# Kernel optimization log

Hardware: AMD Instinct MI355X
Metric: run time of the kernel (lower is better)

Reference implementation:

```python
import jax, jax.numpy as jnp
import numpy as np

N_HEADS = 16
GROUP_SIZE = 4
D_MODEL = 2048
N_GROUPS = N_HEADS // GROUP_SIZE  # 4 KV heads
HEAD_DIM = D_MODEL // N_HEADS     # 128
B, S = 2, 2048


def setup_inputs() -> dict:
    key = jax.random.key(0)
    ks = jax.random.split(key, 10)
    sd = 1.0 / np.sqrt(D_MODEL)
    inp = {
        "x": jax.random.normal(ks[0], (B, S, D_MODEL), dtype=jnp.float32),
        # per-position, per-pair rotation angles (llama-style freqs)
        "rotary_freqs": jax.random.uniform(ks[1], (S, HEAD_DIM // 2), dtype=jnp.float32) * 6.283,
        # weights stored as [in, out] so forward is x @ W + b
        "Wq": jax.random.normal(ks[2], (D_MODEL, D_MODEL), dtype=jnp.float32) * sd,
        "bq": jnp.zeros((D_MODEL,), dtype=jnp.float32),
        "Wk": jax.random.normal(ks[3], (D_MODEL, N_GROUPS * HEAD_DIM), dtype=jnp.float32) * sd,
        "bk": jnp.zeros((N_GROUPS * HEAD_DIM,), dtype=jnp.float32),
        "Wv": jax.random.normal(ks[4], (D_MODEL, N_GROUPS * HEAD_DIM), dtype=jnp.float32) * sd,
        "bv": jnp.zeros((N_GROUPS * HEAD_DIM,), dtype=jnp.float32),
        "Wo": jax.random.normal(ks[5], (D_MODEL, D_MODEL), dtype=jnp.float32) * sd,
        "bo": jnp.zeros((D_MODEL,), dtype=jnp.float32),
    }
    return inp


def _rope(t, cos, sin):
    # t: [B, S, H, head_dim]; cos/sin: [1, S, 1, head_dim//2]
    t2 = t.reshape(t.shape[:-1] + (HEAD_DIM // 2, 2))
    te, to = t2[..., 0], t2[..., 1]
    re = te * cos - to * sin
    ro = te * sin + to * cos
    return jnp.stack([re, ro], axis=-1).reshape(t.shape)


def reference(x, rotary_freqs, Wq, bq, Wk, bk, Wv, bv, Wo, bo):
    Bx, Sx, _ = x.shape
    q = (x @ Wq + bq).reshape(Bx, Sx, N_HEADS, HEAD_DIM)
    k = (x @ Wk + bk).reshape(Bx, Sx, N_GROUPS, HEAD_DIM)
    v = (x @ Wv + bv).reshape(Bx, Sx, N_GROUPS, HEAD_DIM)

    cos = jnp.cos(rotary_freqs)[None, :, None, :]
    sin = jnp.sin(rotary_freqs)[None, :, None, :]
    q = _rope(q, cos, sin)
    k = _rope(k, cos, sin)

    q = q.transpose(0, 2, 1, 3)  # [B, H, S, hd]
    k = k.transpose(0, 2, 1, 3)  # [B, G, S, hd]
    v = v.transpose(0, 2, 1, 3)  # [B, G, S, hd]

    rep = N_HEADS // N_GROUPS
    k = jnp.repeat(k, rep, axis=1)  # repeat_interleave over head dim
    v = jnp.repeat(v, rep, axis=1)

    scores = jnp.einsum("bhsd,bhtd->bhst", q, k) / jnp.sqrt(jnp.float32(HEAD_DIM))
    att = jax.nn.softmax(scores, axis=-1)
    out = jnp.einsum("bhst,bhtd->bhsd", att, v)  # [B, H, S, hd]
    out = out.transpose(0, 2, 1, 3).reshape(Bx, Sx, D_MODEL)
    return out @ Wo + bo
```

## Files before the change

kernel.cpp:

```cpp
#include <hip/hip_runtime.h>
#include <cstdint>
#include <cstddef>

#define NB 2
#define SEQ 2048
#define DMODEL 2048
#define NHEAD 16
#define HDIM 128
#define NGRP 4
#define NKV (NGRP * HDIM)
#define NQKV (DMODEL + 2 * NKV)
#define MROWS (NB * SEQ)
#define QSCALE_LOG2E 0.12751743f

typedef unsigned short u16_t;
typedef unsigned int u32_t;
typedef __bf16 bf16x8 __attribute__((ext_vector_type(8)));
typedef __bf16 bf16x4 __attribute__((ext_vector_type(4)));
typedef float f32x4 __attribute__((ext_vector_type(4)));

static __device__ __forceinline__ u16_t f2bf(float f) {
  u32_t u = __builtin_bit_cast(u32_t, f);
  u32_t r = u + 0x7FFFu + ((u >> 16) & 1u);
  return (u16_t)(r >> 16);
}


__global__ void k_cast_x(const float* __restrict__ x, u16_t* __restrict__ xb) {
  int i = blockIdx.x * 256 + threadIdx.x;
  float4 v = ((const float4*)x)[i];
  uint2 pk;
  pk.x = (u32_t)f2bf(v.x) | ((u32_t)f2bf(v.y) << 16);
  pk.y = (u32_t)f2bf(v.z) | ((u32_t)f2bf(v.w) << 16);
  ((uint2*)xb)[i] = pk;
}

__global__ void k_tables(const float* __restrict__ rf, float* __restrict__ cosT,
                         float* __restrict__ sinT) {
  int i = blockIdx.x * 256 + threadIdx.x;
  float f = rf[i];
  cosT[i] = cosf(f);
  sinT[i] = sinf(f);
}

__global__ void k_bias(const float* __restrict__ bq, const float* __restrict__ bk,
                       const float* __restrict__ bv, float* __restrict__ bqkv) {
  int i = blockIdx.x * 256 + threadIdx.x;
  float v = (i < DMODEL) ? bq[i] : (i < DMODEL + NKV ? bk[i - DMODEL] : bv[i - DMODEL - NKV]);
  bqkv[i] = v;
}

__global__ void k_transpose_cast(const float* __restrict__ W, int N,
                                 u16_t* __restrict__ Wt, int K) {
  __shared__ float tile[64][65];
  int n0 = blockIdx.x * 64, k0 = blockIdx.y * 64;
  int t = threadIdx.x;
#pragma unroll
  for (int pass = 0; pass < 4; ++pass) {
    int slot = pass * 256 + t;
    int r = slot >> 4, c4 = (slot & 15) * 4;
    float4 v = *(const float4*)(W + (size_t)(k0 + r) * N + n0 + c4);
    tile[r][c4] = v.x; tile[r][c4 + 1] = v.y; tile[r][c4 + 2] = v.z; tile[r][c4 + 3] = v.w;
  }
  __syncthreads();
  int nr = t >> 2, seg = t & 3;
  alignas(16) u16_t o[16];
#pragma unroll
  for (int kk = 0; kk < 16; ++kk) o[kk] = f2bf(tile[seg * 16 + kk][nr]);
  u16_t* dst = Wt + (size_t)(n0 + nr) * K + k0 + seg * 16;
  ((int4*)dst)[0] = ((const int4*)o)[0];
  ((int4*)dst)[1] = ((const int4*)o)[1];
}


template <int EPI>
__global__ __launch_bounds__(256, 2) void k_gemm(
    const u16_t* __restrict__ A, const u16_t* __restrict__ Bt, const float* __restrict__ bias,
    float* __restrict__ Cout, u16_t* __restrict__ Qb, u16_t* __restrict__ Kb,
    u16_t* __restrict__ Vt, const float* __restrict__ cosT, const float* __restrict__ sinT,
    int M, int N, int K) {
  __shared__ u16_t lds[16384];
  int tid = threadIdx.x;
  int wid = tid >> 6, lane = tid & 63;
  int l15 = lane & 15, l4 = lane >> 4;
  int wrow = wid >> 1, wcol = wid & 1;

  int m0 = blockIdx.y << 7, n0 = blockIdx.x << 7;

  f32x4 acc[4][4] = {};

  auto stage = [&](int t) {
    u16_t* Al = lds + (t & 1) * 4096;
    u16_t* Bl = lds + 8192 + (t & 1) * 4096;
    int kbase = t * 32;
#pragma unroll
    for (int ss = 0; ss < 2; ++ss) {
      int slot = tid + ss * 256;
      int row = slot >> 2, c = slot & 3;
      int cs = c ^ (row & 3);
      __builtin_amdgcn_global_load_lds(
          (const __attribute__((address_space(1))) u32_t*)(A + (size_t)(m0 + row) * K + kbase + cs * 8),
          (__attribute__((address_space(3))) u32_t*)(Al + slot * 8), 16, 0, 0);
      __builtin_amdgcn_global_load_lds(
          (const __attribute__((address_space(1))) u32_t*)(Bt + (size_t)(n0 + row) * K + kbase + cs * 8),
          (__attribute__((address_space(3))) u32_t*)(Bl + slot * 8), 16, 0, 0);
    }
  };

  stage(0);
  stage(1);

  const int NT = K >> 5;
  for (int t = 0; t < NT; ++t) {
    if (t == NT - 1) {
      asm volatile("s_waitcnt vmcnt(0)" ::: "memory");
    } else {
      asm volatile("s_waitcnt vmcnt(4)" ::: "memory");
    }
    __builtin_amdgcn_s_barrier();
    __builtin_amdgcn_sched_barrier(0);

    const u16_t* Acur = lds + (t & 1) * 4096;
    const u16_t* Bcur = lds + 8192 + (t & 1) * 4096;

    int chunk = l4 ^ (l15 & 3);
    bf16x8 af[4], bfr[4];
#pragma unroll
    for (int i = 0; i < 4; ++i)
      af[i] = *(const bf16x8*)(Acur + (wrow * 64 + i * 16 + l15) * 32 + chunk * 8);
#pragma unroll
    for (int j = 0; j < 4; ++j)
      bfr[j] = *(const bf16x8*)(Bcur + (wcol * 64 + j * 16 + l15) * 32 + chunk * 8);

    __builtin_amdgcn_s_setprio(1);
#pragma unroll
    for (int i = 0; i < 4; ++i)
#pragma unroll
      for (int j = 0; j < 4; ++j)
        acc[i][j] = __builtin_amdgcn_mfma_f32_16x16x32_bf16(af[i], bfr[j], acc[i][j], 0, 0, 0);
    __builtin_amdgcn_s_setprio(0);

    __builtin_amdgcn_sched_barrier(0);
    __builtin_amdgcn_s_barrier();
    __builtin_amdgcn_sched_barrier(0);
    if (t + 2 < NT) stage(t + 2);
  }

  if (EPI == 0) {
#pragma unroll
    for (int j = 0; j < 4; ++j) {
      int n = n0 + wcol * 64 + j * 16 + l15;
      float bs = bias[n];
#pragma unroll
      for (int i = 0; i < 4; ++i) {
        int mbase = m0 + wrow * 64 + i * 16 + l4 * 4;
#pragma unroll
        for (int r = 0; r < 4; ++r)
          Cout[(size_t)(mbase + r) * N + n] = acc[i][j][r] + bs;
      }
    }
  } else {
    bool isV = (n0 >= DMODEL + NKV);
    bool isK = (n0 >= DMODEL) && !isV;
#pragma unroll
    for (int j = 0; j < 4; ++j) {
      int n = n0 + wcol * 64 + j * 16 + l15;
      float bs = bias[n];
      int d = n & (HDIM - 1);
      int p = d >> 1;
      bool evn = !(d & 1);
#pragma unroll
      for (int i = 0; i < 4; ++i) {
        int mbase = m0 + wrow * 64 + i * 16 + l4 * 4;
        if (isV) {
          int g = (n - DMODEL - NKV) >> 7;
          int b = mbase >> 11, s0 = mbase & (SEQ - 1);
          u16_t o[4];
#pragma unroll
          for (int r = 0; r < 4; ++r) o[r] = f2bf(acc[i][j][r] + bs);
          uint2 pk;
          pk.x = (u32_t)o[0] | ((u32_t)o[1] << 16);
          pk.y = (u32_t)o[2] | ((u32_t)o[3] << 16);
          *(uint2*)(Vt + ((size_t)(b * NGRP + g) * HDIM + d) * SEQ + s0) = pk;
        } else {
#pragma unroll
          for (int r = 0; r < 4; ++r) {
            int m = mbase + r;
            int b = m >> 11, s = m & (SEQ - 1);
            float val = acc[i][j][r] + bs;
            float pv = __shfl_xor(val, 1);
            float c = cosT[s * (HDIM / 2) + p];
            float sn = sinT[s * (HDIM / 2) + p];
            float outv = evn ? (val * c - pv * sn) : (pv * sn + val * c);
            if (isK) {
              int g = (n - DMODEL) >> 7;
              Kb[((size_t)(b * NGRP + g) * SEQ + s) * HDIM + d] = f2bf(outv);
            } else {
              int h = n >> 7;
              Qb[((size_t)(b * NHEAD + h) * SEQ + s) * HDIM + d] = f2bf(outv * QSCALE_LOG2E);
            }
          }
        }
      }
    }
  }
}


__global__ __launch_bounds__(256) void k_attn(
    const u16_t* __restrict__ Qb, const u16_t* __restrict__ Kb, const u16_t* __restrict__ Vt,
    u16_t* __restrict__ attn_out) {
  __shared__ u16_t lds[32768];

  int tid = threadIdx.x, wid = tid >> 6, lane = tid & 63;
  int l15 = lane & 15, l4 = lane >> 4;
  int bh = blockIdx.y;
  int b = bh >> 4, h = bh & 15, g = h >> 2;
  int q0 = blockIdx.x * 128;
  const u16_t* Qhead = Qb + (size_t)(b * NHEAD + h) * SEQ * HDIM;
  const u16_t* Khead = Kb + (size_t)(b * NGRP + g) * SEQ * HDIM;
  const u16_t* Vhead = Vt + (size_t)(b * NGRP + g) * HDIM * SEQ;

  bf16x8 qfa[4], qfb[4];
#pragma unroll
  for (int kc = 0; kc < 4; ++kc) {
    qfa[kc] = *(const bf16x8*)(Qhead + (size_t)(q0 + wid * 32 + l15) * HDIM + kc * 32 + l4 * 8);
    qfb[kc] = *(const bf16x8*)(Qhead + (size_t)(q0 + wid * 32 + 16 + l15) * HDIM + kc * 32 + l4 * 8);
  }

  f32x4 oa[8] = {}, ob[8] = {};
  float la = 0.f, lb = 0.f;

  auto stage = [&](int kv0, int bufIdx) {
    u16_t* Kl = lds + bufIdx * 8192;
    u16_t* Vl = lds + 16384 + bufIdx * 8192;
#pragma unroll
    for (int ss = 0; ss < 4; ++ss) {
      int slot = tid + ss * 256;
      int rK = slot >> 4;
      int cK = (slot & 15) ^ ((rK & 3) | (((rK >> 3) & 1) << 2));
      __builtin_amdgcn_global_load_lds(
          (const __attribute__((address_space(1))) u32_t*)(Khead + (size_t)(kv0 + rK) * HDIM + cK * 8),
          (__attribute__((address_space(3))) u32_t*)(Kl + slot * 8), 16, 0, 0);
      int rV = slot >> 3, cV = (slot & 7) ^ (rV & 7);
      __builtin_amdgcn_global_load_lds(
          (const __attribute__((address_space(1))) u32_t*)(Vhead + (size_t)rV * SEQ + kv0 + cV * 8),
          (__attribute__((address_space(3))) u32_t*)(Vl + slot * 8), 16, 0, 0);
    }
  };

  stage(0, 0);

  const int NT = SEQ / 64;
  for (int t = 0; t < NT; ++t) {
    int cur = t & 1;
    if (t + 1 < NT) {
      stage((t + 1) * 64, cur ^ 1);
      asm volatile("s_waitcnt vmcnt(8)" ::: "memory");
    } else {
      asm volatile("s_waitcnt vmcnt(0)" ::: "memory");
    }
    __builtin_amdgcn_s_barrier();
    __builtin_amdgcn_sched_barrier(0);

    const u16_t* Kcur = lds + cur * 8192;
    const u16_t* Vcur = lds + 16384 + cur * 8192;

    f32x4 sa[4] = {}, sb[4] = {};
    __builtin_amdgcn_s_setprio(1);
#pragma unroll
    for (int kc = 0; kc < 4; ++kc) {
#pragma unroll
      for (int kvb = 0; kvb < 4; ++kvb) {
        int row = (l15 >> 2) * 8 + ((kvb & 1) << 2) + (l15 & 3) + ((kvb >> 1) << 5);
        int chunk = ((kc << 2) + l4) ^ (l15 & 7);
        bf16x8 kf = *(const bf16x8*)(Kcur + row * 128 + chunk * 8);
        sa[kvb] = __builtin_amdgcn_mfma_f32_16x16x32_bf16(kf, qfa[kc], sa[kvb], 0, 0, 0);
        sb[kvb] = __builtin_amdgcn_mfma_f32_16x16x32_bf16(kf, qfb[kc], sb[kvb], 0, 0, 0);
      }
    }
    __builtin_amdgcn_s_setprio(0);

    bf16x4 pa[4], pb[4];
#pragma unroll
    for (int kvb = 0; kvb < 4; ++kvb) {
#pragma unroll
      for (int r = 0; r < 4; ++r) {
        float ea = __builtin_amdgcn_exp2f(sa[kvb][r]);
        float eb = __builtin_amdgcn_exp2f(sb[kvb][r]);
        la += ea; lb += eb;
        pa[kvb][r] = (__bf16)ea;
        pb[kvb][r] = (__bf16)eb;
      }
    }

    bf16x8 pfa[2], pfb[2];
#pragma unroll
    for (int kc2 = 0; kc2 < 2; ++kc2) {
      uint2 alo = __builtin_bit_cast(uint2, pa[kc2 * 2]);
      uint2 ahi = __builtin_bit_cast(uint2, pa[kc2 * 2 + 1]);
      uint4 wa; wa.x = alo.x; wa.y = alo.y; wa.z = ahi.x; wa.w = ahi.y;
      pfa[kc2] = __builtin_bit_cast(bf16x8, wa);
      uint2 blo = __builtin_bit_cast(uint2, pb[kc2 * 2]);
      uint2 bhi = __builtin_bit_cast(uint2, pb[kc2 * 2 + 1]);
      uint4 wb; wb.x = blo.x; wb.y = blo.y; wb.z = bhi.x; wb.w = bhi.y;
      pfb[kc2] = __builtin_bit_cast(bf16x8, wb);
    }

    __builtin_amdgcn_s_setprio(1);
#pragma unroll
    for (int kc2 = 0; kc2 < 2; ++kc2) {
#pragma unroll
      for (int dcb = 0; dcb < 8; ++dcb) {
        int chunk = ((kc2 << 2) + l4) ^ (l15 & 7);
        bf16x8 vf = *(const bf16x8*)(Vcur + (dcb * 16 + l15) * 64 + chunk * 8);
        oa[dcb] = __builtin_amdgcn_mfma_f32_16x16x32_bf16(vf, pfa[kc2], oa[dcb], 0, 0, 0);
        ob[dcb] = __builtin_amdgcn_mfma_f32_16x16x32_bf16(vf, pfb[kc2], ob[dcb], 0, 0, 0);
      }
    }
    __builtin_amdgcn_s_setprio(0);

    __builtin_amdgcn_sched_barrier(0);
    __builtin_amdgcn_s_barrier();
  }

  la += __shfl_xor(la, 16); la += __shfl_xor(la, 32);
  lb += __shfl_xor(lb, 16); lb += __shfl_xor(lb, 32);
  float inva = 1.0f / la, invb = 1.0f / lb;

#pragma unroll
  for (int half = 0; half < 2; ++half) {
    u16_t* Owave = lds + half * 8704 + wid * 2176;
    const f32x4* oacc = half ? ob : oa;
    float inv = half ? invb : inva;
#pragma unroll
    for (int dcb = 0; dcb < 8; ++dcb) {
      bf16x4 ov;
#pragma unroll
      for (int r = 0; r < 4; ++r) ov[r] = (__bf16)(oacc[dcb][r] * inv);
      *(uint2*)(Owave + l15 * 136 + dcb * 16 + l4 * 4) = __builtin_bit_cast(uint2, ov);
    }
#pragma unroll
    for (int pass = 0; pass < 4; ++pass) {
      int rowq = pass * 4 + l4;
      int4 v = *(const int4*)(Owave + rowq * 136 + l15 * 8);
      int s = q0 + wid * 32 + half * 16 + rowq;
      *(int4*)(attn_out + ((size_t)(b * SEQ + s)) * DMODEL + h * HDIM + l15 * 8) = v;
    }
  }
}


extern "C" void kernel_launch(void* const* d_in, const int* in_sizes, int n_in,
                              void* d_out, int out_size, void* d_ws, size_t ws_size,
                              hipStream_t stream) {
  (void)in_sizes; (void)n_in; (void)out_size; (void)ws_size;
  const float* x  = (const float*)d_in[0];
  const float* rf = (const float*)d_in[1];
  const float* Wq = (const float*)d_in[2];
  const float* bq = (const float*)d_in[3];
  const float* Wk = (const float*)d_in[4];
  const float* bk = (const float*)d_in[5];
  const float* Wv = (const float*)d_in[6];
  const float* bv = (const float*)d_in[7];
  const float* Wo = (const float*)d_in[8];
  const float* bo = (const float*)d_in[9];
  float* out = (float*)d_out;

  char* ws = (char*)d_ws;
  u16_t* xb    = (u16_t*)ws;  ws += (size_t)MROWS * DMODEL * 2;
  u16_t* Wqkvt = (u16_t*)ws;  ws += (size_t)NQKV * DMODEL * 2;
  u16_t* Wot   = (u16_t*)ws;  ws += (size_t)DMODEL * DMODEL * 2;
  float* bqkv  = (float*)ws;  ws += (size_t)NQKV * 4;
  float* cosT  = (float*)ws;  ws += (size_t)SEQ * (HDIM / 2) * 4;
  float* sinT  = (float*)ws;  ws += (size_t)SEQ * (HDIM / 2) * 4;
  u16_t* Qb    = (u16_t*)ws;  ws += (size_t)NB * NHEAD * SEQ * HDIM * 2;
  u16_t* Kb    = (u16_t*)ws;  ws += (size_t)NB * NGRP * SEQ * HDIM * 2;
  u16_t* Vt    = (u16_t*)ws;  ws += (size_t)NB * NGRP * HDIM * SEQ * 2;
  u16_t* attn  = xb;

  k_cast_x<<<MROWS * DMODEL / 1024, 256, 0, stream>>>(x, xb);
  k_tables<<<SEQ * (HDIM / 2) / 256, 256, 0, stream>>>(rf, cosT, sinT);
  k_bias<<<NQKV / 256, 256, 0, stream>>>(bq, bk, bv, bqkv);

  dim3 tgq(DMODEL / 64, DMODEL / 64);
  dim3 tgk(NKV / 64, DMODEL / 64);
  k_transpose_cast<<<tgq, 256, 0, stream>>>(Wq, DMODEL, Wqkvt, DMODEL);
  k_transpose_cast<<<tgk, 256, 0, stream>>>(Wk, NKV, Wqkvt + (size_t)DMODEL * DMODEL, DMODEL);
  k_transpose_cast<<<tgk, 256, 0, stream>>>(Wv, NKV, Wqkvt + (size_t)(DMODEL + NKV) * DMODEL, DMODEL);
  k_transpose_cast<<<tgq, 256, 0, stream>>>(Wo, DMODEL, Wot, DMODEL);

  k_gemm<1><<<dim3(NQKV / 128, MROWS / 128), 256, 0, stream>>>(
      xb, Wqkvt, bqkv, nullptr, Qb, Kb, Vt, cosT, sinT, MROWS, NQKV, DMODEL);

  dim3 ga(SEQ / 128, NB * NHEAD);
  k_attn<<<ga, 256, 0, stream>>>(Qb, Kb, Vt, attn);

  k_gemm<0><<<dim3(DMODEL / 128, MROWS / 128), 256, 0, stream>>>(
      attn, Wot, bo, out, nullptr, nullptr, nullptr, nullptr, nullptr, MROWS, DMODEL, DMODEL);
}
```

Baseline: 218.0 us.

## Software-pipeline attention loop so QK of next tile overlaps softmax of current

Restructures the attention KV loop into a two-stage software pipeline. The QK^T scores for tile t+1 are computed right after the PV product for tile t, and the exp/pack of the next tile happens before the barrier, so the MFMA work can hide the exp latency. K/V staging for tile t+2 is issued after the end-of-step barrier into the buffer just freed, and the loop is manually unrolled by two to ping-pong the score registers. Launch bounds now request 2 blocks per CU, which caps register use and may cause spills given the extra live score accumulators.

```diff
diff --git a/kernel.cpp b/kernel.cpp
--- a/kernel.cpp
+++ b/kernel.cpp
@@ -207,7 +207,7 @@
 }
 
 
-__global__ __launch_bounds__(256) void k_attn(
+__global__ __launch_bounds__(256, 2) void k_attn(
     const u16_t* __restrict__ Qb, const u16_t* __restrict__ Kb, const u16_t* __restrict__ Vt,
     u16_t* __restrict__ attn_out) {
   __shared__ u16_t lds[32768];
@@ -249,25 +249,8 @@
     }
   };
 
-  stage(0, 0);
-
-  const int NT = SEQ / 64;
-  for (int t = 0; t < NT; ++t) {
-    int cur = t & 1;
-    if (t + 1 < NT) {
-      stage((t + 1) * 64, cur ^ 1);
-      asm volatile("s_waitcnt vmcnt(8)" ::: "memory");
-    } else {
-      asm volatile("s_waitcnt vmcnt(0)" ::: "memory");
-    }
-    __builtin_amdgcn_s_barrier();
-    __builtin_amdgcn_sched_barrier(0);
-
-    const u16_t* Kcur = lds + cur * 8192;
-    const u16_t* Vcur = lds + 16384 + cur * 8192;
-
-    f32x4 sa[4] = {}, sb[4] = {};
-    __builtin_amdgcn_s_setprio(1);
+  auto qk = [&](int bufIdx, f32x4 (&Sa)[4], f32x4 (&Sb)[4]) {
+    const u16_t* Kcur = lds + bufIdx * 8192;
 #pragma unroll
     for (int kc = 0; kc < 4; ++kc) {
 #pragma unroll
@@ -275,26 +258,25 @@
         int row = (l15 >> 2) * 8 + ((kvb & 1) << 2) + (l15 & 3) + ((kvb >> 1) << 5);
         int chunk = ((kc << 2) + l4) ^ (l15 & 7);
         bf16x8 kf = *(const bf16x8*)(Kcur + row * 128 + chunk * 8);
-        sa[kvb] = __builtin_amdgcn_mfma_f32_16x16x32_bf16(kf, qfa[kc], sa[kvb], 0, 0, 0);
-        sb[kvb] = __builtin_amdgcn_mfma_f32_16x16x32_bf16(kf, qfb[kc], sb[kvb], 0, 0, 0);
+        Sa[kvb] = __builtin_amdgcn_mfma_f32_16x16x32_bf16(kf, qfa[kc], Sa[kvb], 0, 0, 0);
+        Sb[kvb] = __builtin_amdgcn_mfma_f32_16x16x32_bf16(kf, qfb[kc], Sb[kvb], 0, 0, 0);
       }
     }
-    __builtin_amdgcn_s_setprio(0);
-
+  };
+
+  auto expand = [&](f32x4 (&Sa)[4], f32x4 (&Sb)[4], bf16x8 (&pfa)[2], bf16x8 (&pfb)[2]) {
     bf16x4 pa[4], pb[4];
 #pragma unroll
     for (int kvb = 0; kvb < 4; ++kvb) {
 #pragma unroll
       for (int r = 0; r < 4; ++r) {
-        float ea = __builtin_amdgcn_exp2f(sa[kvb][r]);
-        float eb = __builtin_amdgcn_exp2f(sb[kvb][r]);
+        float ea = __builtin_amdgcn_exp2f(Sa[kvb][r]);
+        float eb = __builtin_amdgcn_exp2f(Sb[kvb][r]);
         la += ea; lb += eb;
         pa[kvb][r] = (__bf16)ea;
         pb[kvb][r] = (__bf16)eb;
       }
     }
-
-    bf16x8 pfa[2], pfb[2];
 #pragma unroll
     for (int kc2 = 0; kc2 < 2; ++kc2) {
       uint2 alo = __builtin_bit_cast(uint2, pa[kc2 * 2]);
@@ -306,8 +288,10 @@
       uint4 wb; wb.x = blo.x; wb.y = blo.y; wb.z = bhi.x; wb.w = bhi.y;
       pfb[kc2] = __builtin_bit_cast(bf16x8, wb);
     }
-
-    __builtin_amdgcn_s_setprio(1);
+  };
+
+  auto pv = [&](int bufIdx, bf16x8 (&pfa)[2], bf16x8 (&pfb)[2]) {
+    const u16_t* Vcur = lds + 16384 + bufIdx * 8192;
 #pragma unroll
     for (int kc2 = 0; kc2 < 2; ++kc2) {
 #pragma unroll
@@ -318,10 +302,46 @@
         ob[dcb] = __builtin_amdgcn_mfma_f32_16x16x32_bf16(vf, pfb[kc2], ob[dcb], 0, 0, 0);
       }
     }
+  };
+
+  auto step = [&](int t, f32x4 (&Ia)[4], f32x4 (&Ib)[4], f32x4 (&Oa)[4], f32x4 (&Ob)[4]) {
+    bf16x8 pfa[2], pfb[2];
+    expand(Ia, Ib, pfa, pfb);
+    asm volatile("s_waitcnt vmcnt(0)" ::: "memory");
+    __builtin_amdgcn_s_barrier();
+    __builtin_amdgcn_sched_barrier(0);
+#pragma unroll
+    for (int z = 0; z < 4; ++z)
+#pragma unroll
+      for (int r = 0; r < 4; ++r) { Oa[z][r] = 0.f; Ob[z][r] = 0.f; }
+    __builtin_amdgcn_s_setprio(1);
+    pv(t & 1, pfa, pfb);
+    qk((t + 1) & 1, Oa, Ob);
     __builtin_amdgcn_s_setprio(0);
-
     __builtin_amdgcn_sched_barrier(0);
     __builtin_amdgcn_s_barrier();
+    __builtin_amdgcn_sched_barrier(0);
+    if (t + 2 < SEQ / 64) stage((t + 2) * 64, t & 1);
+  };
+
+  f32x4 sA[4] = {}, sB[4] = {}, tA[4], tB[4];
+
+  stage(0, 0);
+  stage(64, 1);
+  asm volatile("s_waitcnt vmcnt(8)" ::: "memory");
+  __builtin_amdgcn_s_barrier();
+  __builtin_amdgcn_sched_barrier(0);
+  qk(0, sA, sB);
+
+  for (int p = 0; p < 15; ++p) {
+    step(2 * p, sA, sB, tA, tB);
+    step(2 * p + 1, tA, tB, sA, sB);
+  }
+  step(30, sA, sB, tA, tB);
+  {
+    bf16x8 pfa[2], pfb[2];
+    expand(tA, tB, pfa, pfb);
+    pv(1, pfa, pfb);
   }
 
   la += __shfl_xor(la, 16); la += __shfl_xor(la, 32);
```

New measurement: 206.3 us. 5.4% less time.
